# Performance work log

Measured on AMD Instinct MI355X. Metric: run time of the kernel, lower is better.

Reference implementation:

```python
import jax, jax.numpy as jnp
import numpy as np

DIM = 1024
HEADS = 16
HEAD_DIM = DIM // HEADS
MLP_HIDDEN = DIM * 4
EPS = 1e-6


def _ln(x):
    # LayerNorm without affine, eps=1e-6
    mu = jnp.mean(x, axis=-1, keepdims=True)
    var = jnp.var(x, axis=-1, keepdims=True)
    return (x - mu) / jnp.sqrt(var + EPS)


def setup_inputs() -> dict:
    key = jax.random.key(0)
    ks = jax.random.split(key, 12)
    B, N = 8, 1024
    s = lambda fan: 1.0 / np.sqrt(fan)
    return {
        "x": jax.random.normal(ks[0], (B, N, DIM), jnp.float32),
        "c": jax.random.normal(ks[1], (B, DIM), jnp.float32),
        "w_qkv": jax.random.normal(ks[2], (DIM, 3 * DIM), jnp.float32) * s(DIM),
        "b_qkv": jnp.zeros((3 * DIM,), jnp.float32),
        "w_proj": jax.random.normal(ks[3], (DIM, DIM), jnp.float32) * s(DIM),
        "b_proj": jnp.zeros((DIM,), jnp.float32),
        "w_mlp1": jax.random.normal(ks[4], (DIM, MLP_HIDDEN), jnp.float32) * s(DIM),
        "b_mlp1": jnp.zeros((MLP_HIDDEN,), jnp.float32),
        "w_mlp2": jax.random.normal(ks[5], (MLP_HIDDEN, DIM), jnp.float32) * s(MLP_HIDDEN),
        "b_mlp2": jnp.zeros((DIM,), jnp.float32),
        "w_ada": jax.random.normal(ks[6], (DIM, 6 * DIM), jnp.float32) * s(DIM),
        "b_ada": jnp.zeros((6 * DIM,), jnp.float32),
    }


def _attention(h, w_qkv, b_qkv, w_proj, b_proj):
    B, N, C = h.shape
    qkv = h @ w_qkv + b_qkv  # [B,N,3C]
    qkv = qkv.reshape(B, N, 3, HEADS, HEAD_DIM)
    q, k, v = qkv[:, :, 0], qkv[:, :, 1], qkv[:, :, 2]  # [B,N,H,Dh]
    scale = HEAD_DIM ** -0.5
    attn = jnp.einsum("bqhd,bkhd->bhqk", q, k) * scale
    attn = jax.nn.softmax(attn, axis=-1)
    o = jnp.einsum("bhqk,bkhd->bqhd", attn, v).reshape(B, N, C)
    return o @ w_proj + b_proj


def reference(x, c, w_qkv, b_qkv, w_proj, b_proj, w_mlp1, b_mlp1, w_mlp2, b_mlp2, w_ada, b_ada):
    mod = (jax.nn.silu(c) @ w_ada + b_ada)[:, None, :]  # [B,1,6D]
    g1, be1, a1, g2, be2, a2 = jnp.split(mod, 6, axis=-1)
    h = _ln(x) * (1.0 + g1) + be1
    x = x + a1 * _attention(h, w_qkv, b_qkv, w_proj, b_proj)
    h = _ln(x) * (1.0 + g2) + be2
    mlp = jax.nn.gelu(h @ w_mlp1 + b_mlp1, approximate=False) @ w_mlp2 + b_mlp2
    return x + a2 * mlp
```

## Files before the change

kernel.cpp:

```cpp
#include <hip/hip_runtime.h>
#include <hip/hip_bf16.h>

#define DIMC 1024
#define SEQ  1024
#define NB   8
#define NH   16
#define HD2  64
#define EPSV 1e-6f

typedef short short8 __attribute__((ext_vector_type(8)));
typedef float floatx4 __attribute__((ext_vector_type(4)));

#define GLOAD_LDS(g, l) \
  __builtin_amdgcn_global_load_lds((const __attribute__((address_space(1))) unsigned int*)(g), \
                                   (__attribute__((address_space(3))) unsigned int*)(l), 16, 0, 0)

__device__ __forceinline__ float bf2f(unsigned short u){
  union { float f; unsigned int i; } v; v.i = ((unsigned int)u) << 16; return v.f;
}
__device__ __forceinline__ unsigned short f2bf(float f){
  union { float f; unsigned int i; } v; v.f = f;
  unsigned int r = v.i + 0x7fffu + ((v.i >> 16) & 1u);
  return (unsigned short)(r >> 16);
}

__device__ __forceinline__ float gelu_f(float v){
  const float z  = fabsf(v) * 0.70710678f;
  const float t  = __builtin_amdgcn_rcpf(fmaf(0.3275911f, z, 1.0f));
  float p = fmaf(t, 1.061405429f, -1.453152027f);
  p = fmaf(t, p, 1.421413741f);
  p = fmaf(t, p, -0.284496736f);
  p = fmaf(t, p, 0.254829592f);
  float erfz = fmaf(-p * t, __expf(-z * z), 1.0f);
  erfz = (v < 0.0f) ? -erfz : erfz;
  return 0.5f * v * (1.0f + erfz);
}

__device__ __forceinline__ void tcvt_body(const float* __restrict__ in,
                                          unsigned short* __restrict__ out,
                                          int K, int N, int bx, int by, int t,
                                          float* shbuf)
{
  const int n0 = bx * 32;
  const int k0 = by * 32;
  const int tx = t & 31;
  const int ty = t >> 5;
#pragma unroll
  for (int i = 0; i < 4; i++)
    shbuf[(ty + i*8) * 33 + tx] = in[(size_t)(k0 + ty + i*8) * N + n0 + tx];
  __syncthreads();
#pragma unroll
  for (int i = 0; i < 4; i++)
    out[(size_t)(n0 + ty + i*8) * K + k0 + tx] = f2bf(shbuf[tx * 33 + ty + i*8]);
}

__global__ __launch_bounds__(256)
void prep_kernel(const float* __restrict__ w_qkv,  unsigned short* __restrict__ wqkv_t,
                 const float* __restrict__ w_proj, unsigned short* __restrict__ wproj_t,
                 const float* __restrict__ w_mlp1, unsigned short* __restrict__ wmlp1_t,
                 const float* __restrict__ w_mlp2, unsigned short* __restrict__ wmlp2_t,
                 const float* __restrict__ c,      const float* __restrict__ w_ada,
                 float* __restrict__ partial)
{
  __shared__ float shbuf[1056];
  const int b = blockIdx.x;
  const int t = threadIdx.x;
  if (b < 3072) {
    tcvt_body(w_qkv, wqkv_t, 1024, 3072, b % 96, b / 96, t, shbuf);
  } else if (b < 4096) {
    const int r = b - 3072;
    tcvt_body(w_proj, wproj_t, 1024, 1024, r % 32, r / 32, t, shbuf);
  } else if (b < 8192) {
    const int r = b - 4096;
    tcvt_body(w_mlp1, wmlp1_t, 1024, 4096, r % 128, r / 128, t, shbuf);
  } else if (b < 12288) {
    const int r = b - 8192;
    tcvt_body(w_mlp2, wmlp2_t, 4096, 1024, r % 32, r / 32, t, shbuf);
  } else {
    const int r = b - 12288;
    const int chunk = r / 24;
    const int col = (r % 24) * 256 + t;
    for (int i = t; i < NB * 128; i += 256) {
      const int bb = i >> 7, k = i & 127;
      const float v = c[bb * DIMC + chunk * 128 + k];
      shbuf[bb * 128 + k] = v / (1.0f + __expf(-v));
    }
    __syncthreads();
    float acc[NB];
#pragma unroll
    for (int bb = 0; bb < NB; bb++) acc[bb] = 0.0f;
#pragma unroll 8
    for (int k = 0; k < 128; k++) {
      const float wv = w_ada[(size_t)(chunk * 128 + k) * 6144 + col];
#pragma unroll
      for (int bb = 0; bb < NB; bb++) acc[bb] = fmaf(shbuf[bb * 128 + k], wv, acc[bb]);
    }
#pragma unroll
    for (int bb = 0; bb < NB; bb++)
      partial[((size_t)chunk * NB + bb) * 6144 + col] = acc[bb];
  }
}

__global__ __launch_bounds__(256)
void ada2_kernel(const float* __restrict__ partial, const float* __restrict__ b_ada,
                 float* __restrict__ mod)
{
  const int i = blockIdx.x * 256 + threadIdx.x;
  const int b = i / 6144, col = i % 6144;
  float s = b_ada[col];
#pragma unroll
  for (int ch = 0; ch < 8; ch++) s += partial[((size_t)ch * NB + b) * 6144 + col];
  mod[i] = s;
}

__global__ __launch_bounds__(256)
void ln_kernel(const float* __restrict__ xin, const float* __restrict__ mod,
               int goff, int boff, unsigned short* __restrict__ hout)
{
  const int row = blockIdx.x;
  const int bb = row >> 10;
  const int t = threadIdx.x;
  const float4 x4 = *((const float4*)(xin + (size_t)row * DIMC) + t);
  const float v0 = x4.x, v1 = x4.y, v2 = x4.z, v3 = x4.w;
  float s  = v0 + v1 + v2 + v3;
  float ss = v0*v0 + v1*v1 + v2*v2 + v3*v3;
#pragma unroll
  for (int off = 32; off > 0; off >>= 1) {
    s  += __shfl_down(s,  off, 64);
    ss += __shfl_down(ss, off, 64);
  }
  __shared__ float red[10];
  const int w = t >> 6;
  if ((t & 63) == 0) { red[w] = s; red[4 + w] = ss; }
  __syncthreads();
  if (t == 0) {
    const float S  = red[0] + red[1] + red[2] + red[3];
    const float SS = red[4] + red[5] + red[6] + red[7];
    const float mu = S * (1.0f / 1024.0f);
    red[8] = mu;
    red[9] = rsqrtf(SS * (1.0f / 1024.0f) - mu * mu + EPSV);
  }
  __syncthreads();
  const float mu = red[8], rstd = red[9];
  const float* mrow = mod + (size_t)bb * 6144;
  const int d = t * 4;
  const float h0 = (v0 - mu) * rstd * (1.0f + mrow[goff + d + 0]) + mrow[boff + d + 0];
  const float h1 = (v1 - mu) * rstd * (1.0f + mrow[goff + d + 1]) + mrow[boff + d + 1];
  const float h2 = (v2 - mu) * rstd * (1.0f + mrow[goff + d + 2]) + mrow[boff + d + 2];
  const float h3 = (v3 - mu) * rstd * (1.0f + mrow[goff + d + 3]) + mrow[boff + d + 3];
  uint2 u;
  u.x = (unsigned)f2bf(h0) | ((unsigned)f2bf(h1) << 16);
  u.y = (unsigned)f2bf(h2) | ((unsigned)f2bf(h3) << 16);
  *((uint2*)(hout + (size_t)row * DIMC + d)) = u;
}

#define MF(a, b, c) __builtin_amdgcn_mfma_f32_16x16x32_bf16(a, b, c, 0, 0, 0)
#define FENCE() asm volatile("" ::: "memory")
#define BARRIER() do { FENCE(); __builtin_amdgcn_s_barrier(); FENCE(); } while (0)

template<int MODE, int BM, int BN>
__global__ __launch_bounds__(512, 2)
void gemm256_kernel(const unsigned short* __restrict__ A,
                    const unsigned short* __restrict__ Bt,
                    const float* __restrict__ bias,
                    void* __restrict__ Cout,
                    const float* __restrict__ resid,
                    const float* __restrict__ mod,
                    int M, int N, int K)
{
  constexpr int NWN = BN / 64;
  constexpr int NWM = 8 / NWN;
  constexpr int NI  = BM / NWM / 16;
  constexpr int AU  = BM / 128;
  constexpr int BU  = BN / 128;

  __shared__ unsigned short As[2][BM * 64];
  __shared__ unsigned short Bs[2][BN * 64];

  const int mT = M / BM;
  const int mb = mT >> 3;
  const int bid = blockIdx.x;
  const int xcd = bid & 7;
  const int local = bid >> 3;
  const int ni = local / mb;
  const int mi = xcd * mb + (local - ni * mb);
  const int m0 = mi * BM, n0 = ni * BN;

  const int tid = threadIdx.x;
  const int w = tid >> 6, lane = tid & 63;
  const int quad = lane >> 4, c16 = lane & 15;
  const int wm = w / NWN, wn = w % NWN;

  const int aRow = (wm * (NI * 16) + c16) * 64;
  const int bRow = (wn * 64 + c16) * 64;
  const int sxz  = (c16 & 7) << 4;
  const int swz0 = ((0  + quad * 16) ^ sxz) >> 1;
  const int swz1 = ((64 + quad * 16) ^ sxz) >> 1;
#define LDA8(cc, i, SW) (*(const short8*)&As[cc][aRow + (i) * 1024 + (SW)])
#define LDB8(cc, j, SW) (*(const short8*)&Bs[cc][bRow + (j) * 1024 + (SW)])

  const int l8 = lane >> 3, lc = lane & 7;
  const int stC = ((lc ^ l8) << 3);
  const int wRowA = w * (BM / 16);
  const int wRowB = w * (BN / 16);
  const unsigned short* aSt = A  + (size_t)(m0 + wRowA + l8) * K + stC;
  const unsigned short* bSt = Bt + (size_t)(n0 + wRowB + l8) * K + stC;
#define STAGE_A(cc, h, kk0) do { \
  _Pragma("unroll") \
  for (int u_ = 0; u_ < AU; u_++) \
    GLOAD_LDS(aSt + (size_t)((h) * (BM/2) + u_*8) * K + (kk0), \
              &As[cc][((h) * (BM/2) + u_*8 + wRowA) * 64]); \
} while (0)
#define STAGE_B(cc, h, kk0) do { \
  _Pragma("unroll") \
  for (int u_ = 0; u_ < BU; u_++) \
    GLOAD_LDS(bSt + (size_t)((h) * (BN/2) + u_*8) * K + (kk0), \
              &Bs[cc][((h) * (BN/2) + u_*8 + wRowB) * 64]); \
} while (0)

  floatx4 acc[NI][4];
#pragma unroll
  for (int i = 0; i < NI; i++)
#pragma unroll
    for (int j = 0; j < 4; j++) acc[i][j] = (floatx4)(0.0f);

#define MMROW(i, aE, aO) do { \
  acc[i][0] = MF(aE, bF00, acc[i][0]); acc[i][0] = MF(aO, bF01, acc[i][0]); \
  acc[i][1] = MF(aE, bF10, acc[i][1]); acc[i][1] = MF(aO, bF11, acc[i][1]); \
  acc[i][2] = MF(aE, bF20, acc[i][2]); acc[i][2] = MF(aO, bF21, acc[i][2]); \
  acc[i][3] = MF(aE, bF30, acc[i][3]); acc[i][3] = MF(aO, bF31, acc[i][3]); \
} while (0)

#define PH_TAIL(i0, i1) do { \
  BARRIER(); \
  asm volatile("s_waitcnt lgkmcnt(0)" ::: "memory"); \
  __builtin_amdgcn_sched_barrier(0); \
  __builtin_amdgcn_s_setprio(1); \
  MMROW(i0, a0, a1); \
  MMROW(i1, a2, a3); \
  __builtin_amdgcn_s_setprio(0); \
} while (0)

#define VMCNT_TAIL(dB_) do { \
  if (dB_) { if constexpr (BU == 1) { asm volatile("s_waitcnt vmcnt(2)" ::: "memory"); } \
             else                   { asm volatile("s_waitcnt vmcnt(4)" ::: "memory"); } } \
  else { asm volatile("s_waitcnt vmcnt(0)" ::: "memory"); } \
} while (0)

#define GROUP4(cc, oo, g) do { \
  const int kA_ = ((g) + 1) << 6; const int kB_ = ((g) + 2) << 6; \
  const bool dA_ = kA_ < K; const bool dB_ = kB_ < K; \
  short8 bF00 = LDB8(cc, 0, swz0), bF01 = LDB8(cc, 0, swz1); \
  short8 bF10 = LDB8(cc, 1, swz0), bF11 = LDB8(cc, 1, swz1); \
  short8 bF20 = LDB8(cc, 2, swz0), bF21 = LDB8(cc, 2, swz1); \
  short8 bF30 = LDB8(cc, 3, swz0), bF31 = LDB8(cc, 3, swz1); \
  short8 a0 = LDA8(cc, 0, swz0), a1 = LDA8(cc, 0, swz1); \
  short8 a2 = LDA8(cc, 1, swz0), a3 = LDA8(cc, 1, swz1); \
  if (dA_) STAGE_A(oo, 0, kA_); \
  PH_TAIL(0, 1); \
  BARRIER(); \
  a0 = LDA8(cc, 2, swz0); a1 = LDA8(cc, 2, swz1); \
  a2 = LDA8(cc, 3, swz0); a3 = LDA8(cc, 3, swz1); \
  if (dA_) STAGE_A(oo, 1, kA_); \
  PH_TAIL(2, 3); \
  BARRIER(); \
  a0 = LDA8(cc, 4, swz0); a1 = LDA8(cc, 4, swz1); \
  a2 = LDA8(cc, 5, swz0); a3 = LDA8(cc, 5, swz1); \
  if (dB_) STAGE_B(cc, 0, kB_); \
  PH_TAIL(4, 5); \
  BARRIER(); \
  a0 = LDA8(cc, 6, swz0); a1 = LDA8(cc, 6, swz1); \
  a2 = LDA8(cc, 7, swz0); a3 = LDA8(cc, 7, swz1); \
  if (dB_) STAGE_B(cc, 1, kB_); \
  PH_TAIL(6, 7); \
  VMCNT_TAIL(dB_); \
  BARRIER(); \
} while (0)

#define GROUP2(cc, oo, g) do { \
  const int kA_ = ((g) + 1) << 6; const int kB_ = ((g) + 2) << 6; \
  const bool dA_ = kA_ < K; const bool dB_ = kB_ < K; \
  short8 bF00 = LDB8(cc, 0, swz0), bF01 = LDB8(cc, 0, swz1); \
  short8 bF10 = LDB8(cc, 1, swz0), bF11 = LDB8(cc, 1, swz1); \
  short8 bF20 = LDB8(cc, 2, swz0), bF21 = LDB8(cc, 2, swz1); \
  short8 bF30 = LDB8(cc, 3, swz0), bF31 = LDB8(cc, 3, swz1); \
  short8 a0 = LDA8(cc, 0, swz0), a1 = LDA8(cc, 0, swz1); \
  short8 a2 = LDA8(cc, 1, swz0), a3 = LDA8(cc, 1, swz1); \
  if (dA_) { STAGE_A(oo, 0, kA_); STAGE_A(oo, 1, kA_); } \
  PH_TAIL(0, 1); \
  BARRIER(); \
  a0 = LDA8(cc, 2, swz0); a1 = LDA8(cc, 2, swz1); \
  a2 = LDA8(cc, 3, swz0); a3 = LDA8(cc, 3, swz1); \
  if (dB_) { STAGE_B(cc, 0, kB_); STAGE_B(cc, 1, kB_); } \
  PH_TAIL(2, 3); \
  VMCNT_TAIL(dB_); \
  BARRIER(); \
} while (0)

  STAGE_B(0, 0, 0);  STAGE_B(0, 1, 0);
  STAGE_A(0, 0, 0);  STAGE_A(0, 1, 0);
  STAGE_B(1, 0, 64); STAGE_B(1, 1, 64);
  if constexpr (BU == 1) { asm volatile("s_waitcnt vmcnt(2)" ::: "memory"); }
  else                   { asm volatile("s_waitcnt vmcnt(4)" ::: "memory"); }
  BARRIER();

  const int T = K >> 6;
  for (int g = 0; g < T; g += 2) {
    if constexpr (BM == 256 && BN == 256) { GROUP4(0, 1, g); GROUP4(1, 0, g + 1); }
    else                                  { GROUP2(0, 1, g); GROUP2(1, 0, g + 1); }
  }

  const int bb = m0 >> 10;
  if (MODE == 0 || MODE == 1) {
    constexpr int EPW = NI * 1024;
    constexpr int WIA = (2 * BM * 64) / EPW;
    unsigned short* eb = (w < WIA)
        ? (unsigned short*)As + w * EPW
        : (unsigned short*)Bs + (w - WIA) * EPW;
#pragma unroll
    for (int j = 0; j < 4; j++) {
      const int col = n0 + wn * 64 + j * 16 + c16;
      const float bv = bias[col];
#pragma unroll
      for (int i = 0; i < NI; i++)
#pragma unroll
        for (int r = 0; r < 4; r++) {
          float v = acc[i][j][r] + bv;
          if (MODE == 1) v = gelu_f(v);
          const int row = i * 16 + quad * 4 + r;
          const int pc8 = (j * 2 + (c16 >> 3)) ^ (row & 7);
          eb[row * 64 + pc8 * 8 + (c16 & 7)] = f2bf(v);
        }
    }
    unsigned short* cw = (unsigned short*)Cout
                       + (size_t)(m0 + wm * (NI * 16)) * N + n0 + wn * 64;
    const int seg = lane & 7;
#pragma unroll
    for (int it = 0; it < NI * 2; it++) {
      const int row = it * 8 + (lane >> 3);
      *(uint4*)(cw + (size_t)row * N + seg * 8) =
          *(const uint4*)&eb[row * 64 + ((seg ^ (row & 7)) * 8)];
    }
  } else {
#pragma unroll
    for (int j = 0; j < 4; j++) {
      const int col = n0 + wn * 64 + j * 16 + c16;
      const float bv = bias[col];
      const float av = mod[(size_t)bb * 6144 + (MODE == 2 ? 2048 : 5120) + col];
#pragma unroll
      for (int i = 0; i < NI; i++) {
        const int rowb = m0 + wm * (NI * 16) + i * 16 + quad * 4;
#pragma unroll
        for (int r = 0; r < 4; r++) {
          const size_t idx = (size_t)(rowb + r) * N + col;
          ((float*)Cout)[idx] = fmaf(av, acc[i][j][r] + bv, resid[idx]);
        }
      }
    }
  }
#undef GROUP4
#undef GROUP2
#undef PH_TAIL
#undef VMCNT_TAIL
#undef MMROW
#undef STAGE_A
#undef STAGE_B
#undef LDA8
#undef LDB8
}

__global__ __launch_bounds__(256, 2)
void fattn_kernel(const unsigned short* __restrict__ qkv, unsigned short* __restrict__ o_out)
{
  __shared__ unsigned short Ks[64][72];
  __shared__ unsigned short Vt[64][72];
  __shared__ unsigned short Pt[4][32][72];

  const int blk = blockIdx.x;
  const int qt = blk & 7;
  const int h  = (blk >> 3) & 15;
  const int bb = blk >> 7;
  const int tid = threadIdx.x;
  const int w = tid >> 6;
  const int lane = tid & 63;
  const int quad = lane >> 4;
  const int c16 = lane & 15;
  const int q0 = qt * 128 + w * 32;

  short8 qf[2][2];
#pragma unroll
  for (int msub = 0; msub < 2; msub++)
#pragma unroll
    for (int kh = 0; kh < 2; kh++) {
      const size_t idx = ((size_t)((bb*SEQ + q0 + msub*16 + c16) * 3 + 0)) * DIMC
                       + h * HD2 + kh * 32 + quad * 8;
      const uint4 u = *(const uint4*)(qkv + idx);
      const unsigned short* pu = (const unsigned short*)&u;
      short8 r;
#pragma unroll
      for (int j = 0; j < 8; j++) r[j] = (short)f2bf(bf2f(pu[j]) * 0.125f);
      qf[msub][kh] = r;
    }

  floatx4 oacc[2][4];
  float lsum[2][4];
#pragma unroll
  for (int msub = 0; msub < 2; msub++) {
#pragma unroll
    for (int r = 0; r < 4; r++) lsum[msub][r] = 0.0f;
#pragma unroll
    for (int d = 0; d < 4; d++) oacc[msub][d] = (floatx4)(0.0f);
  }

  const int tok = tid & 63;
  const int dg = tid >> 6;

  for (int kt = 0; kt < 16; kt++) {
    __syncthreads();
    {
      const size_t base = ((size_t)((bb*SEQ + kt*64 + tok) * 3)) * DIMC + h * HD2 + dg * 16;
      const uint4 ku0 = *(const uint4*)(qkv + base + DIMC);
      const uint4 ku1 = *(const uint4*)(qkv + base + DIMC + 8);
      const uint4 vu0 = *(const uint4*)(qkv + base + 2*DIMC);
      const uint4 vu1 = *(const uint4*)(qkv + base + 2*DIMC + 8);
      *(uint4*)&Ks[tok][dg*16]     = ku0;
      *(uint4*)&Ks[tok][dg*16 + 8] = ku1;
      const unsigned short* vp0 = (const unsigned short*)&vu0;
      const unsigned short* vp1 = (const unsigned short*)&vu1;
#pragma unroll
      for (int j = 0; j < 8; j++) Vt[dg*16 + j][tok] = vp0[j];
#pragma unroll
      for (int j = 0; j < 8; j++) Vt[dg*16 + 8 + j][tok] = vp1[j];
    }
    __syncthreads();

    floatx4 s[2][4];
#pragma unroll
    for (int msub = 0; msub < 2; msub++)
#pragma unroll
      for (int nsub = 0; nsub < 4; nsub++) s[msub][nsub] = (floatx4)(0.0f);
#pragma unroll
    for (int nsub = 0; nsub < 4; nsub++) {
      const short8 kf0 = *(const short8*)&Ks[nsub*16 + c16][quad*8];
      const short8 kf1 = *(const short8*)&Ks[nsub*16 + c16][32 + quad*8];
#pragma unroll
      for (int msub = 0; msub < 2; msub++) {
        s[msub][nsub] = __builtin_amdgcn_mfma_f32_16x16x32_bf16(qf[msub][0], kf0, s[msub][nsub], 0, 0, 0);
        s[msub][nsub] = __builtin_amdgcn_mfma_f32_16x16x32_bf16(qf[msub][1], kf1, s[msub][nsub], 0, 0, 0);
      }
    }

#pragma unroll
    for (int msub = 0; msub < 2; msub++)
#pragma unroll
      for (int nsub = 0; nsub < 4; nsub++)
#pragma unroll
        for (int r = 0; r < 4; r++) {
          const float p = __expf(s[msub][nsub][r] - 8.0f);
          lsum[msub][r] += p;
          Pt[w][msub*16 + quad*4 + r][nsub*16 + c16] = f2bf(p);
        }

    short8 pa[2][2];
#pragma unroll
    for (int msub = 0; msub < 2; msub++) {
      pa[msub][0] = *(const short8*)&Pt[w][msub*16 + c16][quad*8];
      pa[msub][1] = *(const short8*)&Pt[w][msub*16 + c16][32 + quad*8];
    }
#pragma unroll
    for (int dsub = 0; dsub < 4; dsub++) {
      const short8 vf0 = *(const short8*)&Vt[dsub*16 + c16][quad*8];
      const short8 vf1 = *(const short8*)&Vt[dsub*16 + c16][32 + quad*8];
#pragma unroll
      for (int msub = 0; msub < 2; msub++) {
        oacc[msub][dsub] = __builtin_amdgcn_mfma_f32_16x16x32_bf16(pa[msub][0], vf0, oacc[msub][dsub], 0, 0, 0);
        oacc[msub][dsub] = __builtin_amdgcn_mfma_f32_16x16x32_bf16(pa[msub][1], vf1, oacc[msub][dsub], 0, 0, 0);
      }
    }
  }

#pragma unroll
  for (int msub = 0; msub < 2; msub++) {
    float rl[4];
#pragma unroll
    for (int r = 0; r < 4; r++) {
      float t = lsum[msub][r];
#pragma unroll
      for (int xm = 1; xm < 16; xm <<= 1) t += __shfl_xor(t, xm, 64);
      rl[r] = 1.0f / t;
    }
#pragma unroll
    for (int dsub = 0; dsub < 4; dsub++)
#pragma unroll
      for (int r = 0; r < 4; r++) {
        const size_t idx = (size_t)(bb*SEQ + q0 + msub*16 + quad*4 + r) * DIMC
                         + h * HD2 + dsub*16 + c16;
        o_out[idx] = f2bf(oacc[msub][dsub][r] * rl[r]);
      }
  }
}

extern "C" void kernel_launch(void* const* d_in, const int* in_sizes, int n_in,
                              void* d_out, int out_size, void* d_ws, size_t ws_size,
                              hipStream_t stream) {
  const float* x      = (const float*)d_in[0];
  const float* c      = (const float*)d_in[1];
  const float* w_qkv  = (const float*)d_in[2];
  const float* b_qkv  = (const float*)d_in[3];
  const float* w_proj = (const float*)d_in[4];
  const float* b_proj = (const float*)d_in[5];
  const float* w_mlp1 = (const float*)d_in[6];
  const float* b_mlp1 = (const float*)d_in[7];
  const float* w_mlp2 = (const float*)d_in[8];
  const float* b_mlp2 = (const float*)d_in[9];
  const float* w_ada  = (const float*)d_in[10];
  const float* b_ada  = (const float*)d_in[11];

  char* ws = (char*)d_ws;
  float*          mod     = (float*)(ws);
  unsigned short* wqkv_t  = (unsigned short*)(ws + 196608);
  unsigned short* wproj_t = (unsigned short*)(ws + 6488064);
  unsigned short* wmlp1_t = (unsigned short*)(ws + 8585216);
  unsigned short* wmlp2_t = (unsigned short*)(ws + 16973824);
  unsigned short* bufH    = (unsigned short*)(ws + 25362432);
  float*          adapart = (float*)(ws + 25362432);
  unsigned short* qkv     = (unsigned short*)(ws + 42139648);
  unsigned short* hid     = (unsigned short*)(ws + 42139648);
  float*          out     = (float*)d_out;

  const int M = NB * SEQ;

  prep_kernel<<<12480, 256, 0, stream>>>(w_qkv, wqkv_t, w_proj, wproj_t,
                                         w_mlp1, wmlp1_t, w_mlp2, wmlp2_t,
                                         c, w_ada, adapart);
  ada2_kernel<<<192, 256, 0, stream>>>(adapart, b_ada, mod);

  ln_kernel<<<M, 256, 0, stream>>>(x, mod, 0, 1024, bufH);
  gemm256_kernel<0,256,128><<<768, 512, 0, stream>>>(bufH, wqkv_t, b_qkv, qkv, nullptr, nullptr, M, 3072, 1024);
  fattn_kernel<<<1024, 256, 0, stream>>>(qkv, bufH);
  gemm256_kernel<2,256,128><<<256, 512, 0, stream>>>(bufH, wproj_t, b_proj, out, x, mod, M, 1024, 1024);
  ln_kernel<<<M, 256, 0, stream>>>(out, mod, 3072, 4096, bufH);

  const size_t fullHidEnd = 42139648ull + (size_t)M * 4096 * 2;
  if (ws_size >= fullHidEnd) {
    gemm256_kernel<1,256,256><<<512, 512, 0, stream>>>(bufH, wmlp1_t, b_mlp1, hid,
                                                       nullptr, nullptr, M, 4096, 1024);
    gemm256_kernel<3,128,256><<<256, 512, 0, stream>>>(hid, wmlp2_t, b_mlp2, out,
                                                       out, mod, M, 1024, 4096);
  } else {
    for (int half = 0; half < 2; half++) {
      const size_t roff = (size_t)half * 4096;
      gemm256_kernel<1,256,256><<<256, 512, 0, stream>>>(bufH + roff * DIMC, wmlp1_t, b_mlp1, hid,
                                                         nullptr, nullptr, 4096, 4096, 1024);
      gemm256_kernel<3,128,256><<<128, 512, 0, stream>>>(hid, wmlp2_t, b_mlp2, out + roff * DIMC,
                                                         out + roff * DIMC, mod + (size_t)half * 4 * 6144,
                                                         4096, 1024, 4096);
    }
  }
}
```

Before: 482.3 us.

## Widen weight transpose tiles and prefetch next K/V tile in attention

The weight transpose-and-convert step now uses 64x64 tiles with float4 loads and packed 4-element bf16 stores, cutting the prep grid from 12480 to 3264 blocks and making global accesses wider. The flash attention loop now loads the next K/V tile into registers right after the LDS barrier, so global load latency overlaps with the MFMA and softmax work on the current tile. This costs extra live registers in the attention kernel, which could lower occupancy.

Measured after the change: 486.8 us. No clear change (+0.9%).

```diff
diff --git a/kernel.cpp b/kernel.cpp
--- a/kernel.cpp
+++ b/kernel.cpp
@@ -36,22 +36,29 @@
   return 0.5f * v * (1.0f + erfz);
 }
 
-__device__ __forceinline__ void tcvt_body(const float* __restrict__ in,
-                                          unsigned short* __restrict__ out,
-                                          int K, int N, int bx, int by, int t,
-                                          float* shbuf)
+__device__ __forceinline__ void tcvt64_body(const float* __restrict__ in,
+                                            unsigned short* __restrict__ out,
+                                            int K, int N, int bx, int by, int t,
+                                            float* sh)
 {
-  const int n0 = bx * 32;
-  const int k0 = by * 32;
-  const int tx = t & 31;
-  const int ty = t >> 5;
-#pragma unroll
-  for (int i = 0; i < 4; i++)
-    shbuf[(ty + i*8) * 33 + tx] = in[(size_t)(k0 + ty + i*8) * N + n0 + tx];
+  const int n0 = bx * 64, k0 = by * 64;
+  const int tr = t >> 4;
+  const int tc = (t & 15) * 4;
+#pragma unroll
+  for (int i = 0; i < 4; i++) {
+    const float4 v = *(const float4*)(in + (size_t)(k0 + tr + i*16) * N + n0 + tc);
+    float* d = &sh[(tr + i*16) * 65 + tc];
+    d[0] = v.x; d[1] = v.y; d[2] = v.z; d[3] = v.w;
+  }
   __syncthreads();
 #pragma unroll
-  for (int i = 0; i < 4; i++)
-    out[(size_t)(n0 + ty + i*8) * K + k0 + tx] = f2bf(shbuf[tx * 33 + ty + i*8]);
+  for (int i = 0; i < 4; i++) {
+    const int nr = tr + i*16;
+    uint2 u;
+    u.x = (unsigned)f2bf(sh[(tc+0)*65 + nr]) | ((unsigned)f2bf(sh[(tc+1)*65 + nr]) << 16);
+    u.y = (unsigned)f2bf(sh[(tc+2)*65 + nr]) | ((unsigned)f2bf(sh[(tc+3)*65 + nr]) << 16);
+    *(uint2*)(out + (size_t)(n0 + nr) * K + k0 + tc) = u;
+  }
 }
 
 __global__ __launch_bounds__(256)
@@ -62,22 +69,22 @@
                  const float* __restrict__ c,      const float* __restrict__ w_ada,
                  float* __restrict__ partial)
 {
-  __shared__ float shbuf[1056];
+  __shared__ float shbuf[64 * 65];
   const int b = blockIdx.x;
   const int t = threadIdx.x;
-  if (b < 3072) {
-    tcvt_body(w_qkv, wqkv_t, 1024, 3072, b % 96, b / 96, t, shbuf);
-  } else if (b < 4096) {
+  if (b < 768) {
+    tcvt64_body(w_qkv, wqkv_t, 1024, 3072, b % 48, b / 48, t, shbuf);
+  } else if (b < 1024) {
+    const int r = b - 768;
+    tcvt64_body(w_proj, wproj_t, 1024, 1024, r % 16, r / 16, t, shbuf);
+  } else if (b < 2048) {
+    const int r = b - 1024;
+    tcvt64_body(w_mlp1, wmlp1_t, 1024, 4096, r % 64, r / 64, t, shbuf);
+  } else if (b < 3072) {
+    const int r = b - 2048;
+    tcvt64_body(w_mlp2, wmlp2_t, 4096, 1024, r % 16, r / 16, t, shbuf);
+  } else {
     const int r = b - 3072;
-    tcvt_body(w_proj, wproj_t, 1024, 1024, r % 32, r / 32, t, shbuf);
-  } else if (b < 8192) {
-    const int r = b - 4096;
-    tcvt_body(w_mlp1, wmlp1_t, 1024, 4096, r % 128, r / 128, t, shbuf);
-  } else if (b < 12288) {
-    const int r = b - 8192;
-    tcvt_body(w_mlp2, wmlp2_t, 4096, 1024, r % 32, r / 32, t, shbuf);
-  } else {
-    const int r = b - 12288;
     const int chunk = r / 24;
     const int col = (r % 24) * 256 + t;
     for (int i = t; i < NB * 128; i += 256) {
@@ -415,16 +422,20 @@
   const int tok = tid & 63;
   const int dg = tid >> 6;
 
+  uint4 ku0, ku1, vu0, vu1;
+  {
+    const size_t base = ((size_t)((bb*SEQ + tok) * 3)) * DIMC + h * HD2 + dg * 16;
+    ku0 = *(const uint4*)(qkv + base + DIMC);
+    ku1 = *(const uint4*)(qkv + base + DIMC + 8);
+    vu0 = *(const uint4*)(qkv + base + 2*DIMC);
+    vu1 = *(const uint4*)(qkv + base + 2*DIMC + 8);
+  }
+
   for (int kt = 0; kt < 16; kt++) {
     __syncthreads();
+    *(uint4*)&Ks[tok][dg*16]     = ku0;
+    *(uint4*)&Ks[tok][dg*16 + 8] = ku1;
     {
-      const size_t base = ((size_t)((bb*SEQ + kt*64 + tok) * 3)) * DIMC + h * HD2 + dg * 16;
-      const uint4 ku0 = *(const uint4*)(qkv + base + DIMC);
-      const uint4 ku1 = *(const uint4*)(qkv + base + DIMC + 8);
-      const uint4 vu0 = *(const uint4*)(qkv + base + 2*DIMC);
-      const uint4 vu1 = *(const uint4*)(qkv + base + 2*DIMC + 8);
-      *(uint4*)&Ks[tok][dg*16]     = ku0;
-      *(uint4*)&Ks[tok][dg*16 + 8] = ku1;
       const unsigned short* vp0 = (const unsigned short*)&vu0;
       const unsigned short* vp1 = (const unsigned short*)&vu1;
 #pragma unroll
@@ -433,6 +444,13 @@
       for (int j = 0; j < 8; j++) Vt[dg*16 + 8 + j][tok] = vp1[j];
     }
     __syncthreads();
+    if (kt < 15) {
+      const size_t base = ((size_t)((bb*SEQ + (kt+1)*64 + tok) * 3)) * DIMC + h * HD2 + dg * 16;
+      ku0 = *(const uint4*)(qkv + base + DIMC);
+      ku1 = *(const uint4*)(qkv + base + DIMC + 8);
+      vu0 = *(const uint4*)(qkv + base + 2*DIMC);
+      vu1 = *(const uint4*)(qkv + base + 2*DIMC + 8);
+    }
 
     floatx4 s[2][4];
 #pragma unroll
@@ -530,9 +548,9 @@
 
   const int M = NB * SEQ;
 
-  prep_kernel<<<12480, 256, 0, stream>>>(w_qkv, wqkv_t, w_proj, wproj_t,
-                                         w_mlp1, wmlp1_t, w_mlp2, wmlp2_t,
-                                         c, w_ada, adapart);
+  prep_kernel<<<3264, 256, 0, stream>>>(w_qkv, wqkv_t, w_proj, wproj_t,
+                                        w_mlp1, wmlp1_t, w_mlp2, wmlp2_t,
+                                        c, w_ada, adapart);
   ada2_kernel<<<192, 256, 0, stream>>>(adapart, b_ada, mod);
 
   ln_kernel<<<M, 256, 0, stream>>>(x, mod, 0, 1024, bufH);
```
